# Kernel optimization log

Hardware: AMD Instinct MI355X
Metric: run time of the kernel (lower is better)

The kernel has to match this reference:

```python
import jax, jax.numpy as jnp
import numpy as np

B, T, D, P, NP = 32, 512, 512, 200, 8
RADIUS = 3
TEMP = 1.0
DIRECTION = 'right'
NEG = -100000.0
EPS_NORM = 1e-12


def setup_inputs() -> dict:
    key = jax.random.key(0)
    k1, k2, k3 = jax.random.split(key, 3)
    return {
        "x": jax.random.normal(k1, (B, T, D), dtype=jnp.float32),
        "timeline_mask": jnp.ones((B, T), dtype=jnp.float32),
        "prototype_vectors": jax.random.uniform(k2, (P, D, NP), dtype=jnp.float32),
        "patch_select": jax.random.normal(k3, (1, P, NP), dtype=jnp.float32),
    }


def _l2norm(v, axis):
    return v / jnp.maximum(jnp.linalg.norm(v, axis=axis, keepdims=True), EPS_NORM)


def reference(x, timeline_mask, prototype_vectors, patch_select):
    # --- subpatch_dist ---
    xn = _l2norm(x, axis=-1)                       # (B, T, D)
    pn = _l2norm(prototype_vectors, axis=1)        # (P, D, n_p)
    dist_all = jnp.einsum('btd,pdi->bpti', xn, pn)  # (B, P, T, n_p)

    # timeline mask
    tm = timeline_mask[:, None, :, None]
    dist_all = dist_all * tm + (1.0 - tm) * NEG

    dt = dist_all.dtype
    b, p, t, n_p = dist_all.shape
    ar_t = jnp.arange(t)

    mask_act = jnp.ones((b, p, t), dt)
    mask_subpatch = jnp.ones((b, p, n_p), dt)
    mask_all = jnp.ones((b, p, t, n_p), dt)
    adjacent = jnp.ones((b, p, t), dt)

    ids_list, vals_list, ev_list = [], [], []
    # greedy iterative max-select over the n_p subpatches (sequential dependency)
    for it in range(n_p):
        dm = dist_all + (1.0 - mask_all * adjacent[..., None]) * NEG
        max_subs = dm.max(axis=2)                   # (B, P, n_p) best score per subpatch
        max_subs_id = jnp.argmax(dm, axis=2)        # (B, P, n_p) best event per subpatch
        max_sub_act = max_subs.max(axis=-1)         # (B, P)
        sub_id = jnp.argmax(max_subs, axis=-1)      # (B, P) chosen subpatch
        event_id = jnp.take_along_axis(max_subs_id, sub_id[..., None], axis=2)[..., 0]  # (B, P)

        neigh = (jnp.abs(ar_t[None, None, :] - event_id[..., None]) <= RADIUS).astype(dt)
        if it > 0:
            if DIRECTION == 'right':
                dmask = (ar_t[None, None, :] > event_id[..., None]).astype(dt)
            else:
                dmask = (ar_t[None, None, :] < event_id[..., None]).astype(dt)
            neigh = neigh * dmask
        adjacent = neigh

        # suppress chosen event and chosen subpatch (scatter_ 0 == multiply by 1-onehot)
        mask_act = mask_act * (1.0 - jax.nn.one_hot(event_id, t, dtype=dt))
        mask_subpatch = mask_subpatch * (1.0 - jax.nn.one_hot(sub_id, n_p, dtype=dt))
        mask_all = mask_all * mask_act[..., None] * mask_subpatch[:, :, None, :]

        ids_list.append(sub_id)
        vals_list.append(max_sub_act)
        ev_list.append(event_id.astype(dt))

    subpatch_ids = jnp.stack(ids_list, axis=-1)   # (B, P, n_p) int
    values = jnp.stack(vals_list, axis=-1)        # (B, P, n_p)
    indices = jnp.stack(ev_list, axis=-1)         # (B, P, n_p) float, matches torch cat promotion

    order = jnp.argsort(subpatch_ids, axis=-1)    # unique ids -> deterministic permutation
    values_r = jnp.take_along_axis(values, order, axis=-1)
    indices_r = jnp.take_along_axis(indices, order, axis=-1)

    slots = jax.nn.sigmoid(patch_select * TEMP)           # (1, P, n_p)
    factor = slots.sum(-1, keepdims=True) + 1e-10
    values_slot = values_r * (slots * n_p / factor)
    max_activation_slots = values_slot.sum(-1)            # (B, P)
    min_distances = n_p - max_activation_slots
    return (max_activation_slots, min_distances, indices_r)
```

## Files before the change

### kernel.cpp

```cpp
#include <hip/hip_runtime.h>
#include <hip/hip_bf16.h>
#include <hip/hip_fp16.h>
#include <math.h>

#define B_    32
#define T_    512
#define D_    512
#define P_    200
#define NP_   8
#define N_TOT 1600
#define NEG_  (-100000.0f)
#define LO_SCALE 2048.0f
#define LO_INV   (1.0f/2048.0f)

typedef __attribute__((ext_vector_type(8))) _Float16 f16x8;
typedef __attribute__((ext_vector_type(4))) _Float16 f16x4;
typedef __attribute__((ext_vector_type(4))) float   f32x4;
typedef unsigned long long u64;

#define GLL16(gp, lp) __builtin_amdgcn_global_load_lds( \
    (const __attribute__((address_space(1))) void*)(gp), \
    (__attribute__((address_space(3))) void*)(lp), 16, 0, 0)

__device__ __forceinline__ float wave_reduce_sum(float v) {
#pragma unroll
  for (int off = 32; off; off >>= 1) v += __shfl_xor(v, off, 64);
  return v;
}

__device__ __forceinline__ unsigned ordf(float f) {
  unsigned u = __float_as_uint(f);
  return (u & 0x80000000u) ? ~u : (u | 0x80000000u);
}
__device__ __forceinline__ float deco(unsigned o) {
  unsigned u = (o & 0x80000000u) ? (o ^ 0x80000000u) : ~o;
  return __uint_as_float(u);
}
__device__ __forceinline__ u64 packvk(float v, int key) {
  return ((u64)ordf(v) << 32) | (u64)(4095 - key);
}

__global__ void init_slots(u64* s) {
  int i = blockIdx.x * 256 + threadIdx.x;
  if (i < 2 * B_ * P_) s[i] = 0ULL;
}

__global__ __launch_bounds__(256) void norm_x_kernel(const float* __restrict__ x,
                                                     _Float16* __restrict__ xh,
                                                     _Float16* __restrict__ xl) {
  int row  = blockIdx.x * 4 + (threadIdx.x >> 6);
  int lane = threadIdx.x & 63;
  const float* xr = x + (size_t)row * D_;
  float4 v0 = *(const float4*)(xr + lane * 4);
  float4 v1 = *(const float4*)(xr + 256 + lane * 4);
  float s = v0.x*v0.x + v0.y*v0.y + v0.z*v0.z + v0.w*v0.w
          + v1.x*v1.x + v1.y*v1.y + v1.z*v1.z + v1.w*v1.w;
  s = wave_reduce_sum(s);
  float dn = fmaxf(sqrtf(s), 1e-12f);
  float f[8] = {v0.x/dn, v0.y/dn, v0.z/dn, v0.w/dn, v1.x/dn, v1.y/dn, v1.z/dn, v1.w/dn};
  f16x4 h0, h1, l0, l1;
#pragma unroll
  for (int j = 0; j < 4; j++) {
    h0[j] = (_Float16)f[j];
    l0[j] = (_Float16)((f[j] - (float)h0[j]) * LO_SCALE);
    h1[j] = (_Float16)f[4 + j];
    l1[j] = (_Float16)((f[4 + j] - (float)h1[j]) * LO_SCALE);
  }
  size_t base = (size_t)row * D_;
  *(f16x4*)(xh + base + lane * 4)       = h0;
  *(f16x4*)(xh + base + 256 + lane * 4) = h1;
  *(f16x4*)(xl + base + lane * 4)       = l0;
  *(f16x4*)(xl + base + 256 + lane * 4) = l1;
}

__global__ __launch_bounds__(256) void norm_w_kernel(const float* __restrict__ proto,
                                                     _Float16* __restrict__ wh,
                                                     _Float16* __restrict__ wl) {
  int n    = blockIdx.x * 4 + (threadIdx.x >> 6);
  int lane = threadIdx.x & 63;
  int p = n >> 3, i = n & 7;
  float v[8];
  float s = 0.f;
#pragma unroll
  for (int k = 0; k < 8; k++) {
    int d = k * 64 + lane;
    v[k] = proto[((size_t)p * D_ + d) * NP_ + i];
    s += v[k] * v[k];
  }
  s = wave_reduce_sum(s);
  float dn = fmaxf(sqrtf(s), 1e-12f);
  size_t base = (size_t)n * D_;
#pragma unroll
  for (int k = 0; k < 8; k++) {
    float f = v[k] / dn;
    _Float16 h = (_Float16)f;
    wh[base + k * 64 + lane] = h;
    wl[base + k * 64 + lane] = (_Float16)((f - (float)h) * LO_SCALE);
  }
}

__global__ __launch_bounds__(256, 2) void gemm_mfma(
    const _Float16* __restrict__ XH, const _Float16* __restrict__ XL,
    const _Float16* __restrict__ WH, const _Float16* __restrict__ WL,
    const float* __restrict__ tm, float* __restrict__ dist,
    u64* __restrict__ rawslot, u64* __restrict__ qslot) {
  __shared__ _Float16 lds[16384];
  const int b  = blockIdx.z;
  const int n0 = blockIdx.y * 128;
  const int t0 = blockIdx.x * 128;
  const int tid = threadIdx.x;
  const int w = tid >> 6, l = tid & 63;
  const int fr = l & 15;
  const int lk = (l >> 4) * 8;

  const _Float16* pHi[4]; const _Float16* pLo[4];
  int dstoff;
  {
    int H = w >> 1;
    if ((w & 1) == 0) {
#pragma unroll
      for (int m = 0; m < 4; m++) {
        int row = n0 + H * 64 + m * 16 + fr;
        if (row > N_TOT - 1) row = N_TOT - 1;
        pHi[m] = WH + (size_t)row * D_ + lk;
        pLo[m] = WL + (size_t)row * D_ + lk;
      }
      dstoff = H * 2048;
    } else {
#pragma unroll
      for (int m = 0; m < 4; m++) {
        int col = t0 + H * 64 + m * 16 + fr;
        pHi[m] = XH + ((size_t)b * T_ + col) * D_ + lk;
        pLo[m] = XL + ((size_t)b * T_ + col) * D_ + lk;
      }
      dstoff = 8192 + H * 2048;
    }
  }

#define STAGE(kk) do { \
    _Float16* dh = &lds[dstoff]; \
    _Float16* dl = dh + 4096; \
    GLL16(pHi[0] + (kk), dh);        GLL16(pHi[1] + (kk), dh + 512); \
    GLL16(pHi[2] + (kk), dh + 1024); GLL16(pHi[3] + (kk), dh + 1536); \
    GLL16(pLo[0] + (kk), dl);        GLL16(pLo[1] + (kk), dl + 512); \
    GLL16(pLo[2] + (kk), dl + 1024); GLL16(pLo[3] + (kk), dl + 1536); \
  } while (0)

  const int aB = (w >> 1) * 2048;
  const int xB = 8192 + (w & 1) * 2048;

  f32x4 acch[4][4], accc[4][4];
#pragma unroll
  for (int m = 0; m < 4; m++)
#pragma unroll
    for (int n = 0; n < 4; n++) { acch[m][n] = (f32x4)0.0f; accc[m][n] = (f32x4)0.0f; }

  for (int kt = 0; kt < 16; ++kt) {
    STAGE(kt * 32);
    __syncthreads();
    f16x8 ah[4], al[4], bh[4], bl[4];
#pragma unroll
    for (int m = 0; m < 4; m++) {
      ah[m] = *(const f16x8*)&lds[aB + m * 512 + l * 8];
      al[m] = *(const f16x8*)&lds[aB + 4096 + m * 512 + l * 8];
    }
#pragma unroll
    for (int n = 0; n < 4; n++) {
      bh[n] = *(const f16x8*)&lds[xB + n * 512 + l * 8];
      bl[n] = *(const f16x8*)&lds[xB + 4096 + n * 512 + l * 8];
    }
#pragma unroll
    for (int m = 0; m < 4; m++)
#pragma unroll
      for (int n = 0; n < 4; n++) {
        acch[m][n] = __builtin_amdgcn_mfma_f32_16x16x32_f16(ah[m], bh[n], acch[m][n], 0, 0, 0);
        accc[m][n] = __builtin_amdgcn_mfma_f32_16x16x32_f16(ah[m], bl[n], accc[m][n], 0, 0, 0);
        accc[m][n] = __builtin_amdgcn_mfma_f32_16x16x32_f16(al[m], bh[n], accc[m][n], 0, 0, 0);
      }
    __syncthreads();
  }

  const int fq = l >> 4;
  u64 pm[4], qm[4];
#pragma unroll
  for (int m = 0; m < 4; m++) { pm[m] = 0ULL; qm[m] = 0ULL; }
#pragma unroll
  for (int n = 0; n < 4; n++) {
    int col = t0 + (w & 1) * 64 + n * 16 + fr;
    float tmc = tm[b * T_ + col];
#pragma unroll
    for (int m = 0; m < 4; m++) {
      int nb = n0 + (w >> 1) * 64 + m * 16 + fq * 4;
#pragma unroll
      for (int r = 0; r < 4; r++) {
        int nr = nb + r;
        if (nr < N_TOT) {
          float v = acch[m][n][r] + accc[m][n][r] * LO_INV;
          v = v * tmc + (1.0f - tmc) * NEG_;
          dist[((size_t)b * N_TOT + nr) * T_ + col] = v;
          int key = ((fq * 4 + r) & 7) * T_ + col;
          u64 pk = packvk(v, key);
          if (pk > pm[m]) pm[m] = pk;
          u64 qk = packvk(v + NEG_, key);
          if (qk > qm[m]) qm[m] = qk;
        }
      }
    }
  }
#pragma unroll
  for (int m = 0; m < 4; m++) {
#pragma unroll
    for (int off = 1; off <= 16; off <<= 1) {
      u64 o1 = __shfl_xor(pm[m], off, 64); if (o1 > pm[m]) pm[m] = o1;
      u64 o2 = __shfl_xor(qm[m], off, 64); if (o2 > qm[m]) qm[m] = o2;
    }
  }
  if ((l & 31) == 0) {
    int h = l >> 5;
#pragma unroll
    for (int m = 0; m < 4; m++) {
      int p = (n0 >> 3) + ((w >> 1) * 8) + m * 2 + h;
      if (p < P_) {
        atomicMax(&rawslot[b * P_ + p], pm[m]);
        atomicMax(&qslot[b * P_ + p], qm[m]);
      }
    }
  }
#undef STAGE
}

__global__ __launch_bounds__(256) void select_kernel(const float* __restrict__ dist,
                                                     const u64* __restrict__ rawslot,
                                                     const u64* __restrict__ qslot,
                                                     const float* __restrict__ tmg,
                                                     const float* __restrict__ psel,
                                                     float* __restrict__ out) {
  int w = threadIdx.x >> 6, lane = threadIdx.x & 63;
  int pair = blockIdx.x * 4 + w;
  int b = pair / P_, p = pair % P_;
  const float* dbase = dist + ((size_t)b * N_TOT + p * NP_) * T_;

  bool okt = true;
#pragma unroll
  for (int c = 0; c < 8; c++) okt = okt && (tmg[b * T_ + c * 64 + lane] == 1.0f);
  bool tmones = (__ballot(okt) == ~0ULL);

  u64 rs = rawslot[pair], qs = qslot[pair];
  float rv = deco((unsigned)(rs >> 32)); int rkey = 4095 - (int)(rs & 0xFFFFu);
  float qv = deco((unsigned)(qs >> 32)); int qkey = 4095 - (int)(qs & 0xFFFFu);

  float valh[8]; int evh[8], sidh[8];
#pragma unroll
  for (int k = 0; k < 8; k++) { valh[k] = 0.f; evh[k] = -1; sidh[k] = 0; }
  unsigned msub = 0xFFu;
  int e_last = 0;

  for (int it = 0; it < 8; ++it) {
    float bv; int bkey;
    if (tmones) {
      if (it == 0) { bv = rv; bkey = rkey; }
      else {
        int i = lane >> 3, widx = lane & 7;
        int tw, nw;
        if (it == 1) { tw = e_last - 3 + widx; nw = 7; }
        else         { tw = e_last + 1 + widx; nw = 3; }
        bool valid = (widx < nw) && (tw >= 0) && (tw < T_) && (((msub >> i) & 1u) != 0u);
#pragma unroll
        for (int k = 0; k < 8; k++) if (tw == evh[k]) valid = false;
        float v  = valid ? dbase[(size_t)i * T_ + tw] : -3.0e38f;
        int  key = valid ? (i * T_ + tw) : 0x7FFFFFFF;
#pragma unroll
        for (int off = 32; off; off >>= 1) {
          float ov = __shfl_xor(v, off, 64);
          int  ok2 = __shfl_xor(key, off, 64);
          if (ov > v || (ov == v && ok2 < key)) { v = ov; key = ok2; }
        }
        if (v > -2.9e38f) { bv = v; bkey = key; }
        else              { bv = qv; bkey = qkey; }
      }
    } else {
      float lv = -3.0e38f; int lkey = 0x7FFFFFFF;
      for (int i = 0; i < 8; i++) {
        bool sub_ok = ((msub >> i) & 1u) != 0u;
        const float* row = dbase + (size_t)i * T_;
        float4 u0 = *(const float4*)(row + lane * 8);
        float4 u1 = *(const float4*)(row + lane * 8 + 4);
        float uv[8] = {u0.x, u0.y, u0.z, u0.w, u1.x, u1.y, u1.z, u1.w};
#pragma unroll
        for (int j = 0; j < 8; j++) {
          int t = lane * 8 + j;
          bool act = sub_ok;
          if (it > 0) {
            int dt = t - e_last;
            act = act && (dt <= 3) && (dt >= -3);
            if (it > 1) act = act && (dt > 0);
          }
#pragma unroll
          for (int k = 0; k < 8; k++) if (t == evh[k]) act = false;
          float dm = act ? uv[j] : (uv[j] + NEG_);
          if (dm > lv) { lv = dm; lkey = i * T_ + t; }
        }
      }
#pragma unroll
      for (int off = 32; off; off >>= 1) {
        float ov = __shfl_xor(lv, off, 64);
        int  ok2 = __shfl_xor(lkey, off, 64);
        if (ov > lv || (ov == lv && ok2 < lkey)) { lv = ov; lkey = ok2; }
      }
      bv = lv; bkey = lkey;
    }
    int bi = bkey >> 9, bt = bkey & (T_ - 1);
#pragma unroll
    for (int k = 0; k < 8; k++) {
      if (it == k) { valh[k] = bv; evh[k] = bt; sidh[k] = bi; }
    }
    msub &= ~(1u << bi);
    e_last = bt;
  }

  if (lane == 0) {
    int ord[8]; unsigned used = 0;
#pragma unroll
    for (int j = 0; j < 8; j++) {
      int bk = 1 << 30, bi2 = 0;
#pragma unroll
      for (int k = 0; k < 8; k++)
        if (!((used >> k) & 1u)) { int key = sidh[k] * 8 + k; if (key < bk) { bk = key; bi2 = k; } }
      ord[j] = bi2; used |= 1u << bi2;
    }
    float slots[8]; float ssum = 0.f;
#pragma unroll
    for (int i = 0; i < 8; i++) {
      slots[i] = 1.0f / (1.0f + expf(-psel[p * NP_ + i]));
      ssum += slots[i];
    }
    float fac = ssum + 1e-10f;
    float acc = 0.f;
    float vr[8]; float er[8];
#pragma unroll
    for (int j = 0; j < 8; j++) {
      float vv = 0.f, ee = 0.f;
#pragma unroll
      for (int k = 0; k < 8; k++) if (ord[j] == k) { vv = valh[k]; ee = (float)evh[k]; }
      vr[j] = vv; er[j] = ee;
    }
#pragma unroll
    for (int j = 0; j < 8; j++) acc += vr[j] * (slots[j] * 8.0f / fac);
    int bp = b * P_ + p;
    out[bp] = acc;
    out[B_ * P_ + bp] = 8.0f - acc;
#pragma unroll
    for (int j = 0; j < 8; j++) out[2 * B_ * P_ + bp * 8 + j] = er[j];
  }
}

extern "C" void kernel_launch(void* const* d_in, const int* in_sizes, int n_in,
                              void* d_out, int out_size, void* d_ws, size_t ws_size,
                              hipStream_t stream) {
  const float* x     = (const float*)d_in[0];
  const float* tm    = (const float*)d_in[1];
  const float* proto = (const float*)d_in[2];
  const float* psel  = (const float*)d_in[3];
  float* out = (float*)d_out;

  char* wsb = (char*)d_ws;
  _Float16* XH = (_Float16*)wsb;
  _Float16* XL = (_Float16*)(wsb + 16777216u);
  _Float16* WH = (_Float16*)(wsb + 2u * 16777216u);
  _Float16* WL = (_Float16*)(wsb + 2u * 16777216u + 1638400u);
  float*   dist = (float*)(wsb + 2u * 16777216u + 2u * 1638400u);
  u64*  rawslot = (u64*)(wsb + 141688832u);
  u64*  qslot   = rawslot + B_ * P_;

  init_slots<<<dim3(50), 256, 0, stream>>>(rawslot);
  norm_x_kernel<<<dim3(B_ * T_ / 4), 256, 0, stream>>>(x, XH, XL);
  norm_w_kernel<<<dim3(N_TOT / 4), 256, 0, stream>>>(proto, WH, WL);
  gemm_mfma<<<dim3(T_ / 128, (N_TOT + 127) / 128, B_), 256, 0, stream>>>(
      XH, XL, WH, WL, tm, dist, rawslot, qslot);
  select_kernel<<<dim3(B_ * P_ / 4), 256, 0, stream>>>(dist, rawslot, qslot, tm, psel, out);
}
```

Before: 265.4 us.

## Coalesce GEMM global-to-LDS staging with row-major tiles and fold slot init into norm kernel

The GEMM's global_load_lds staging is reorganized so each lane loads a contiguous 16-byte chunk where four consecutive lanes cover one 64-byte row segment, instead of the old per-fragment pattern that fetched strided 16-byte pieces across 16 rows. LDS becomes a plain row-major [128][32] tile, and MFMA fragments are read from it with computed row offsets. Separately, the init_slots launch is removed and slot zeroing is done by block 0 of norm_w_kernel, saving one kernel launch. The new LDS read pattern, with a 64-byte row stride, may cause bank conflicts on the fragment reads.

```diff
diff --git a/kernel.cpp b/kernel.cpp
--- a/kernel.cpp
+++ b/kernel.cpp
@@ -38,11 +38,6 @@
 }
 __device__ __forceinline__ u64 packvk(float v, int key) {
   return ((u64)ordf(v) << 32) | (u64)(4095 - key);
-}
-
-__global__ void init_slots(u64* s) {
-  int i = blockIdx.x * 256 + threadIdx.x;
-  if (i < 2 * B_ * P_) s[i] = 0ULL;
 }
 
 __global__ __launch_bounds__(256) void norm_x_kernel(const float* __restrict__ x,
@@ -75,7 +70,11 @@
 
 __global__ __launch_bounds__(256) void norm_w_kernel(const float* __restrict__ proto,
                                                      _Float16* __restrict__ wh,
-                                                     _Float16* __restrict__ wl) {
+                                                     _Float16* __restrict__ wl,
+                                                     u64* __restrict__ slotbuf) {
+  if (blockIdx.x == 0) {
+    for (int i = threadIdx.x; i < 2 * B_ * P_; i += 256) slotbuf[i] = 0ULL;
+  }
   int n    = blockIdx.x * 4 + (threadIdx.x >> 6);
   int lane = threadIdx.x & 63;
   int p = n >> 3, i = n & 7;
@@ -104,50 +103,34 @@
     const _Float16* __restrict__ WH, const _Float16* __restrict__ WL,
     const float* __restrict__ tm, float* __restrict__ dist,
     u64* __restrict__ rawslot, u64* __restrict__ qslot) {
-  __shared__ _Float16 lds[16384];
+  __shared__ _Float16 lds[4 * 128 * 32];
   const int b  = blockIdx.z;
   const int n0 = blockIdx.y * 128;
   const int t0 = blockIdx.x * 128;
   const int tid = threadIdx.x;
   const int w = tid >> 6, l = tid & 63;
-  const int fr = l & 15;
-  const int lk = (l >> 4) * 8;
-
-  const _Float16* pHi[4]; const _Float16* pLo[4];
-  int dstoff;
-  {
-    int H = w >> 1;
-    if ((w & 1) == 0) {
-#pragma unroll
-      for (int m = 0; m < 4; m++) {
-        int row = n0 + H * 64 + m * 16 + fr;
-        if (row > N_TOT - 1) row = N_TOT - 1;
-        pHi[m] = WH + (size_t)row * D_ + lk;
-        pLo[m] = WL + (size_t)row * D_ + lk;
-      }
-      dstoff = H * 2048;
-    } else {
-#pragma unroll
-      for (int m = 0; m < 4; m++) {
-        int col = t0 + H * 64 + m * 16 + fr;
-        pHi[m] = XH + ((size_t)b * T_ + col) * D_ + lk;
-        pLo[m] = XL + ((size_t)b * T_ + col) * D_ + lk;
-      }
-      dstoff = 8192 + H * 2048;
-    }
-  }
-
-#define STAGE(kk) do { \
-    _Float16* dh = &lds[dstoff]; \
-    _Float16* dl = dh + 4096; \
-    GLL16(pHi[0] + (kk), dh);        GLL16(pHi[1] + (kk), dh + 512); \
-    GLL16(pHi[2] + (kk), dh + 1024); GLL16(pHi[3] + (kk), dh + 1536); \
-    GLL16(pLo[0] + (kk), dl);        GLL16(pLo[1] + (kk), dl + 512); \
-    GLL16(pLo[2] + (kk), dl + 1024); GLL16(pLo[3] + (kk), dl + 1536); \
-  } while (0)
-
-  const int aB = (w >> 1) * 2048;
-  const int xB = 8192 + (w & 1) * 2048;
+
+  int c0 = (w * 2 + 0) * 64 + l;
+  int c1 = (w * 2 + 1) * 64 + l;
+  int r0 = c0 >> 2, kc0 = (c0 & 3) * 8;
+  int r1 = c1 >> 2, kc1 = (c1 & 3) * 8;
+  int an0 = n0 + r0; if (an0 > N_TOT - 1) an0 = N_TOT - 1;
+  int an1 = n0 + r1; if (an1 > N_TOT - 1) an1 = N_TOT - 1;
+  const _Float16* wh0 = WH + (size_t)an0 * D_ + kc0;
+  const _Float16* wh1 = WH + (size_t)an1 * D_ + kc1;
+  const _Float16* wl0 = WL + (size_t)an0 * D_ + kc0;
+  const _Float16* wl1 = WL + (size_t)an1 * D_ + kc1;
+  const _Float16* xh0 = XH + ((size_t)b * T_ + t0 + r0) * D_ + kc0;
+  const _Float16* xh1 = XH + ((size_t)b * T_ + t0 + r1) * D_ + kc1;
+  const _Float16* xl0 = XL + ((size_t)b * T_ + t0 + r0) * D_ + kc0;
+  const _Float16* xl1 = XL + ((size_t)b * T_ + t0 + r1) * D_ + kc1;
+  _Float16* ldAh = lds +     0 + (w * 2) * 512;
+  _Float16* ldAl = lds +  4096 + (w * 2) * 512;
+  _Float16* ldXh = lds +  8192 + (w * 2) * 512;
+  _Float16* ldXl = lds + 12288 + (w * 2) * 512;
+
+  const int wn = (w >> 1) * 64, wtf = (w & 1) * 64;
+  const int fr = l & 15, fq = l >> 4;
 
   f32x4 acch[4][4], accc[4][4];
 #pragma unroll
@@ -156,18 +139,24 @@
     for (int n = 0; n < 4; n++) { acch[m][n] = (f32x4)0.0f; accc[m][n] = (f32x4)0.0f; }
 
   for (int kt = 0; kt < 16; ++kt) {
-    STAGE(kt * 32);
+    const int k0 = kt * 32;
+    GLL16(wh0 + k0, ldAh); GLL16(wh1 + k0, ldAh + 512);
+    GLL16(wl0 + k0, ldAl); GLL16(wl1 + k0, ldAl + 512);
+    GLL16(xh0 + k0, ldXh); GLL16(xh1 + k0, ldXh + 512);
+    GLL16(xl0 + k0, ldXl); GLL16(xl1 + k0, ldXl + 512);
     __syncthreads();
     f16x8 ah[4], al[4], bh[4], bl[4];
 #pragma unroll
     for (int m = 0; m < 4; m++) {
-      ah[m] = *(const f16x8*)&lds[aB + m * 512 + l * 8];
-      al[m] = *(const f16x8*)&lds[aB + 4096 + m * 512 + l * 8];
+      int ro = (wn + m * 16 + fr) * 32 + fq * 8;
+      ah[m] = *(const f16x8*)&lds[ro];
+      al[m] = *(const f16x8*)&lds[4096 + ro];
     }
 #pragma unroll
     for (int n = 0; n < 4; n++) {
-      bh[n] = *(const f16x8*)&lds[xB + n * 512 + l * 8];
-      bl[n] = *(const f16x8*)&lds[xB + 4096 + n * 512 + l * 8];
+      int ro = (wtf + n * 16 + fr) * 32 + fq * 8;
+      bh[n] = *(const f16x8*)&lds[8192 + ro];
+      bl[n] = *(const f16x8*)&lds[12288 + ro];
     }
 #pragma unroll
     for (int m = 0; m < 4; m++)
@@ -180,17 +169,16 @@
     __syncthreads();
   }
 
-  const int fq = l >> 4;
   u64 pm[4], qm[4];
 #pragma unroll
   for (int m = 0; m < 4; m++) { pm[m] = 0ULL; qm[m] = 0ULL; }
 #pragma unroll
   for (int n = 0; n < 4; n++) {
-    int col = t0 + (w & 1) * 64 + n * 16 + fr;
+    int col = t0 + wtf + n * 16 + fr;
     float tmc = tm[b * T_ + col];
 #pragma unroll
     for (int m = 0; m < 4; m++) {
-      int nb = n0 + (w >> 1) * 64 + m * 16 + fq * 4;
+      int nb = n0 + wn + m * 16 + fq * 4;
 #pragma unroll
       for (int r = 0; r < 4; r++) {
         int nr = nb + r;
@@ -226,7 +214,6 @@
       }
     }
   }
-#undef STAGE
 }
 
 __global__ __launch_bounds__(256) void select_kernel(const float* __restrict__ dist,
@@ -372,9 +359,8 @@
   u64*  rawslot = (u64*)(wsb + 141688832u);
   u64*  qslot   = rawslot + B_ * P_;
 
-  init_slots<<<dim3(50), 256, 0, stream>>>(rawslot);
   norm_x_kernel<<<dim3(B_ * T_ / 4), 256, 0, stream>>>(x, XH, XL);
-  norm_w_kernel<<<dim3(N_TOT / 4), 256, 0, stream>>>(proto, WH, WL);
+  norm_w_kernel<<<dim3(N_TOT / 4), 256, 0, stream>>>(proto, WH, WL, rawslot);
   gemm_mfma<<<dim3(T_ / 128, (N_TOT + 127) / 128, B_), 256, 0, stream>>>(
       XH, XL, WH, WL, tm, dist, rawslot, qslot);
   select_kernel<<<dim3(B_ * P_ / 4), 256, 0, stream>>>(dist, rawslot, qslot, tm, psel, out);
```

New measurement: 231.4 us. -12.8%, faster.
